# Performance work log

Hardware: AMD Instinct MI355X
Metric: run time of the kernel (lower is better)

The kernel has to match this reference:

```python
import jax, jax.numpy as jnp
import numpy as np

N_NODES = 100000
N_EDGES = 3200000
IN_C, HID_C, OUT_C = 64, 64, 32


def setup_inputs() -> dict:
    key = jax.random.key(0)
    ks = jax.random.split(key, 8)
    x = jax.random.normal(ks[0], (N_NODES, IN_C), dtype=jnp.float32)
    edge_index = jax.random.randint(ks[1], (2, N_EDGES), 0, N_NODES, dtype=jnp.int64)
    s1 = 1.0 / np.sqrt(IN_C)
    s2 = 1.0 / np.sqrt(HID_C)
    W1l = jax.random.uniform(ks[2], (IN_C, HID_C), jnp.float32, -s1, s1)
    b1l = jnp.zeros((HID_C,), jnp.float32)
    W1r = jax.random.uniform(ks[3], (IN_C, HID_C), jnp.float32, -s1, s1)
    W2l = jax.random.uniform(ks[4], (HID_C, OUT_C), jnp.float32, -s2, s2)
    b2l = jnp.zeros((OUT_C,), jnp.float32)
    W2r = jax.random.uniform(ks[5], (HID_C, OUT_C), jnp.float32, -s2, s2)
    return {"x": x, "edge_index": edge_index, "W1l": W1l, "b1l": b1l,
            "W1r": W1r, "W2l": W2l, "b2l": b2l, "W2r": W2r}


def _sage_conv(x, src, dst, Wl, bl, Wr):
    # mean-aggregate source features onto destination nodes
    msg = x[src]                                              # [E, d] gather
    summed = jax.ops.segment_sum(msg, dst, num_segments=N_NODES)
    deg = jax.ops.segment_sum(jnp.ones((src.shape[0],), x.dtype), dst,
                              num_segments=N_NODES)
    agg = summed / jnp.maximum(deg, 1.0)[:, None]             # [N, d]
    return agg @ Wl + bl + x @ Wr                             # lin_l(agg)+lin_r(x)


def reference(x, edge_index, W1l, b1l, W1r, W2l, b2l, W2r):
    src, dst = edge_index[0], edge_index[1]
    h = jax.nn.relu(_sage_conv(x, src, dst, W1l, b1l, W1r))
    # dropout is identity in eval mode
    return _sage_conv(h, src, dst, W2l, b2l, W2r)
```

## Files before the change

### kernel.cpp

```cpp
#include <hip/hip_runtime.h>
#include <hip/hip_bf16.h>

#define N_NODES 100000
#define N_EDGES 3200000
#define NBKT 391
#define BKT_CAP 10240

typedef __hip_bfloat16 bf16;
typedef unsigned int uint;
typedef __attribute__((ext_vector_type(8))) short bf16x8;
typedef __attribute__((ext_vector_type(4))) float f32x4;

__device__ __forceinline__ float b2f(bf16 v) { return __bfloat162float(v); }

__device__ __forceinline__ float bits2f(unsigned short w) {
    union { unsigned short u; bf16 b; } c;
    c.u = w;
    return __bfloat162float(c.b);
}
__device__ __forceinline__ unsigned short f2bits(float f) {
    return (unsigned short)(__float_as_uint(f) >> 16);
}
__device__ __forceinline__ unsigned short f2bf_bits(float f) {
    bf16 b = __float2bfloat16(f);
    unsigned short u;
    __builtin_memcpy(&u, &b, 2);
    return u;
}

__device__ __forceinline__ int get_idx(const void* ei, long long pos, int is64) {
    if (is64) return (int)((const long long*)ei)[pos];
    return ((const int*)ei)[pos];
}
__device__ __forceinline__ float get_f(const void* p, long long pos, int isbf) {
    if (isbf) return b2f(((const bf16*)p)[pos]);
    return ((const float*)p)[pos];
}

__global__ void detect_kernel(const void* __restrict__ x,
                              const void* __restrict__ ei,
                              int* __restrict__ flags) {
    int lane = threadIdx.x;
    const unsigned short* xw = (const unsigned short*)x;
    float v = bits2f(xw[2 * lane]);
    bool plaus = (v == v) && fabsf(v) > 1e-3f && fabsf(v) < 1e2f;
    unsigned long long m1 = __ballot(plaus);
    const int* iw = (const int*)ei;
    bool z = (iw[2 * lane + 1] == 0);
    unsigned long long m2 = __ballot(z);
    if (lane == 0) {
        flags[0] = (__popcll(m1) >= 32) ? 1 : 0;
        flags[1] = (__popcll(m2) == 64) ? 1 : 0;
    }
}

__global__ __launch_bounds__(256) void scatterA_kernel(
    const void* __restrict__ ei, int* __restrict__ bucket_cursor,
    uint* __restrict__ bucket_data, const int* __restrict__ flags) {
    __shared__ int lhist[NBKT];
    __shared__ int lbase[NBKT];
    int is64 = flags[1];
    int t = threadIdx.x;
    int chunk0 = blockIdx.x * 8192;
    int dreg[32];

    for (int i = t; i < NBKT; i += 256) lhist[i] = 0;
    __syncthreads();
#pragma unroll
    for (int j = 0; j < 32; j++) {
        int e = chunk0 + j * 256 + t;
        int d = -1;
        if (e < N_EDGES) {
            d = get_idx(ei, (long long)N_EDGES + e, is64);
            atomicAdd(&lhist[d >> 8], 1);
        }
        dreg[j] = d;
    }
    __syncthreads();
    for (int i = t; i < NBKT; i += 256) {
        int c = lhist[i];
        lbase[i] = c ? atomicAdd(&bucket_cursor[i], c) : 0;
        lhist[i] = 0;
    }
    __syncthreads();
#pragma unroll
    for (int j = 0; j < 32; j++) {
        int e = chunk0 + j * 256 + t;
        int d = dreg[j];
        if (d >= 0) {
            int s = get_idx(ei, e, is64);
            int b = d >> 8;
            int o = lbase[b] + atomicAdd(&lhist[b], 1);
            if (o < BKT_CAP)
                bucket_data[(long long)b * BKT_CAP + o] = ((uint)(d & 255) << 17) | (uint)s;
        }
    }
}

__global__ void scanBuckets_kernel(const int* __restrict__ cnt,
                                   int* __restrict__ base) {
    __shared__ int buf[512];
    int t = threadIdx.x;
    int v = (t < NBKT) ? cnt[t] : 0;
    buf[t] = v;
    __syncthreads();
    for (int off = 1; off < 512; off <<= 1) {
        int add = (t >= off) ? buf[t - off] : 0;
        __syncthreads();
        buf[t] += add;
        __syncthreads();
    }
    if (t < NBKT) base[t] = buf[t] - v;
}

__global__ __launch_bounds__(256) void csrB_kernel(
    const int* __restrict__ bucket_cnt, const int* __restrict__ bucket_base,
    const uint* __restrict__ bucket_data, int* __restrict__ csr_src,
    int* __restrict__ row_start) {
    __shared__ int lh[256];
    __shared__ int buf[256];
    int b = blockIdx.x;
    int t = threadIdx.x;
    int cnt = bucket_cnt[b];
    if (cnt > BKT_CAP) cnt = BKT_CAP;
    int base = bucket_base[b];
    const uint* bd = bucket_data + (long long)b * BKT_CAP;

    lh[t] = 0;
    __syncthreads();
    for (int i = t; i < cnt; i += 256) atomicAdd(&lh[bd[i] >> 17], 1);
    __syncthreads();
    int v = lh[t];
    buf[t] = v;
    __syncthreads();
    for (int off = 1; off < 256; off <<= 1) {
        int add = (t >= off) ? buf[t - off] : 0;
        __syncthreads();
        buf[t] += add;
        __syncthreads();
    }
    int excl = buf[t] - v;
    int g = (b << 8) + t;
    if (g < N_NODES) row_start[g] = base + excl;
    lh[t] = excl;
    __syncthreads();
    for (int i = t; i < cnt; i += 256) {
        uint e = bd[i];
        int o = atomicAdd(&lh[e >> 17], 1);
        csr_src[base + o] = (int)(e & 0x1FFFFu);
    }
    if (b == 0 && t == 0) row_start[N_NODES] = N_EDGES;
}

__global__ __launch_bounds__(256) void gather1_kernel(
    const void* __restrict__ x, const int* __restrict__ row_start,
    const int* __restrict__ csr_src, bf16* __restrict__ aggbuf,
    const int* __restrict__ flags) {
    int isbf = flags[0];
    int t = threadIdx.x;
    int lane = t & 63;
    int gw = (blockIdx.x * 256 + t) >> 6;
    int nw = (gridDim.x * 256) >> 6;
    int e8 = lane >> 3, q8 = lane & 7;
    int e4 = lane >> 4, q16 = lane & 15;
    const uint4* xr4 = (const uint4*)x;

    for (int p = gw; p * 2 < N_NODES; p += nw) {
        int na = p * 2, nb = p * 2 + 1;
        int sa = row_start[na], ea = row_start[na + 1];
        int sb = row_start[nb], eb = row_start[nb + 1];
        int da = ea - sa, db = eb - sb;
        int maxd = max(da, db);
        float accA[8] = {0, 0, 0, 0, 0, 0, 0, 0};
        float accB[8] = {0, 0, 0, 0, 0, 0, 0, 0};
        float avA = 0.0f, avB = 0.0f;
        if (isbf) {
            for (int off = 0; off < maxd; off += 32) {
                int iA0 = sa + off + e8, iA1 = iA0 + 8, iA2 = iA0 + 16, iA3 = iA0 + 24;
                int iB0 = sb + off + e8, iB1 = iB0 + 8, iB2 = iB0 + 16, iB3 = iB0 + 24;
                int sA0 = (iA0 < ea) ? csr_src[iA0] : -1;
                int sA1 = (iA1 < ea) ? csr_src[iA1] : -1;
                int sA2 = (iA2 < ea) ? csr_src[iA2] : -1;
                int sA3 = (iA3 < ea) ? csr_src[iA3] : -1;
                int sB0 = (iB0 < eb) ? csr_src[iB0] : -1;
                int sB1 = (iB1 < eb) ? csr_src[iB1] : -1;
                int sB2 = (iB2 < eb) ? csr_src[iB2] : -1;
                int sB3 = (iB3 < eb) ? csr_src[iB3] : -1;
                uint4 vA0 = {0,0,0,0}, vA1 = {0,0,0,0}, vA2 = {0,0,0,0}, vA3 = {0,0,0,0};
                uint4 vB0 = {0,0,0,0}, vB1 = {0,0,0,0}, vB2 = {0,0,0,0}, vB3 = {0,0,0,0};
                if (sA0 >= 0) vA0 = xr4[sA0 * 8 + q8];
                if (sA1 >= 0) vA1 = xr4[sA1 * 8 + q8];
                if (sA2 >= 0) vA2 = xr4[sA2 * 8 + q8];
                if (sA3 >= 0) vA3 = xr4[sA3 * 8 + q8];
                if (sB0 >= 0) vB0 = xr4[sB0 * 8 + q8];
                if (sB1 >= 0) vB1 = xr4[sB1 * 8 + q8];
                if (sB2 >= 0) vB2 = xr4[sB2 * 8 + q8];
                if (sB3 >= 0) vB3 = xr4[sB3 * 8 + q8];
                accA[0] += __uint_as_float(vA0.x << 16) + __uint_as_float(vA1.x << 16)
                         + __uint_as_float(vA2.x << 16) + __uint_as_float(vA3.x << 16);
                accA[1] += __uint_as_float(vA0.x & 0xffff0000u) + __uint_as_float(vA1.x & 0xffff0000u)
                         + __uint_as_float(vA2.x & 0xffff0000u) + __uint_as_float(vA3.x & 0xffff0000u);
                accA[2] += __uint_as_float(vA0.y << 16) + __uint_as_float(vA1.y << 16)
                         + __uint_as_float(vA2.y << 16) + __uint_as_float(vA3.y << 16);
                accA[3] += __uint_as_float(vA0.y & 0xffff0000u) + __uint_as_float(vA1.y & 0xffff0000u)
                         + __uint_as_float(vA2.y & 0xffff0000u) + __uint_as_float(vA3.y & 0xffff0000u);
                accA[4] += __uint_as_float(vA0.z << 16) + __uint_as_float(vA1.z << 16)
                         + __uint_as_float(vA2.z << 16) + __uint_as_float(vA3.z << 16);
                accA[5] += __uint_as_float(vA0.z & 0xffff0000u) + __uint_as_float(vA1.z & 0xffff0000u)
                         + __uint_as_float(vA2.z & 0xffff0000u) + __uint_as_float(vA3.z & 0xffff0000u);
                accA[6] += __uint_as_float(vA0.w << 16) + __uint_as_float(vA1.w << 16)
                         + __uint_as_float(vA2.w << 16) + __uint_as_float(vA3.w << 16);
                accA[7] += __uint_as_float(vA0.w & 0xffff0000u) + __uint_as_float(vA1.w & 0xffff0000u)
                         + __uint_as_float(vA2.w & 0xffff0000u) + __uint_as_float(vA3.w & 0xffff0000u);
                accB[0] += __uint_as_float(vB0.x << 16) + __uint_as_float(vB1.x << 16)
                         + __uint_as_float(vB2.x << 16) + __uint_as_float(vB3.x << 16);
                accB[1] += __uint_as_float(vB0.x & 0xffff0000u) + __uint_as_float(vB1.x & 0xffff0000u)
                         + __uint_as_float(vB2.x & 0xffff0000u) + __uint_as_float(vB3.x & 0xffff0000u);
                accB[2] += __uint_as_float(vB0.y << 16) + __uint_as_float(vB1.y << 16)
                         + __uint_as_float(vB2.y << 16) + __uint_as_float(vB3.y << 16);
                accB[3] += __uint_as_float(vB0.y & 0xffff0000u) + __uint_as_float(vB1.y & 0xffff0000u)
                         + __uint_as_float(vB2.y & 0xffff0000u) + __uint_as_float(vB3.y & 0xffff0000u);
                accB[4] += __uint_as_float(vB0.z << 16) + __uint_as_float(vB1.z << 16)
                         + __uint_as_float(vB2.z << 16) + __uint_as_float(vB3.z << 16);
                accB[5] += __uint_as_float(vB0.z & 0xffff0000u) + __uint_as_float(vB1.z & 0xffff0000u)
                         + __uint_as_float(vB2.z & 0xffff0000u) + __uint_as_float(vB3.z & 0xffff0000u);
                accB[6] += __uint_as_float(vB0.w << 16) + __uint_as_float(vB1.w << 16)
                         + __uint_as_float(vB2.w << 16) + __uint_as_float(vB3.w << 16);
                accB[7] += __uint_as_float(vB0.w & 0xffff0000u) + __uint_as_float(vB1.w & 0xffff0000u)
                         + __uint_as_float(vB2.w & 0xffff0000u) + __uint_as_float(vB3.w & 0xffff0000u);
            }
#pragma unroll
            for (int mm = 8; mm <= 32; mm <<= 1)
#pragma unroll
                for (int k = 0; k < 8; k++) {
                    accA[k] += __shfl_xor(accA[k], mm, 64);
                    accB[k] += __shfl_xor(accB[k], mm, 64);
                }
#pragma unroll
            for (int k = 0; k < 8; k++) {
                float vA = __shfl(accA[k], lane >> 3, 64);
                float vB = __shfl(accB[k], lane >> 3, 64);
                avA = ((lane & 7) == k) ? vA : avA;
                avB = ((lane & 7) == k) ? vB : avB;
            }
        } else {
            const uint4* xf = (const uint4*)x;
            for (int off = 0; off < maxd; off += 16) {
                int iA0 = sa + off + e4, iA1 = iA0 + 4, iA2 = iA0 + 8, iA3 = iA0 + 12;
                int iB0 = sb + off + e4, iB1 = iB0 + 4, iB2 = iB0 + 8, iB3 = iB0 + 12;
                int sA0 = (iA0 < ea) ? csr_src[iA0] : -1;
                int sA1 = (iA1 < ea) ? csr_src[iA1] : -1;
                int sA2 = (iA2 < ea) ? csr_src[iA2] : -1;
                int sA3 = (iA3 < ea) ? csr_src[iA3] : -1;
                int sB0 = (iB0 < eb) ? csr_src[iB0] : -1;
                int sB1 = (iB1 < eb) ? csr_src[iB1] : -1;
                int sB2 = (iB2 < eb) ? csr_src[iB2] : -1;
                int sB3 = (iB3 < eb) ? csr_src[iB3] : -1;
                uint4 vA0 = {0,0,0,0}, vA1 = {0,0,0,0}, vA2 = {0,0,0,0}, vA3 = {0,0,0,0};
                uint4 vB0 = {0,0,0,0}, vB1 = {0,0,0,0}, vB2 = {0,0,0,0}, vB3 = {0,0,0,0};
                if (sA0 >= 0) vA0 = xf[sA0 * 16 + q16];
                if (sA1 >= 0) vA1 = xf[sA1 * 16 + q16];
                if (sA2 >= 0) vA2 = xf[sA2 * 16 + q16];
                if (sA3 >= 0) vA3 = xf[sA3 * 16 + q16];
                if (sB0 >= 0) vB0 = xf[sB0 * 16 + q16];
                if (sB1 >= 0) vB1 = xf[sB1 * 16 + q16];
                if (sB2 >= 0) vB2 = xf[sB2 * 16 + q16];
                if (sB3 >= 0) vB3 = xf[sB3 * 16 + q16];
                accA[0] += __uint_as_float(vA0.x) + __uint_as_float(vA1.x)
                         + __uint_as_float(vA2.x) + __uint_as_float(vA3.x);
                accA[1] += __uint_as_float(vA0.y) + __uint_as_float(vA1.y)
                         + __uint_as_float(vA2.y) + __uint_as_float(vA3.y);
                accA[2] += __uint_as_float(vA0.z) + __uint_as_float(vA1.z)
                         + __uint_as_float(vA2.z) + __uint_as_float(vA3.z);
                accA[3] += __uint_as_float(vA0.w) + __uint_as_float(vA1.w)
                         + __uint_as_float(vA2.w) + __uint_as_float(vA3.w);
                accB[0] += __uint_as_float(vB0.x) + __uint_as_float(vB1.x)
                         + __uint_as_float(vB2.x) + __uint_as_float(vB3.x);
                accB[1] += __uint_as_float(vB0.y) + __uint_as_float(vB1.y)
                         + __uint_as_float(vB2.y) + __uint_as_float(vB3.y);
                accB[2] += __uint_as_float(vB0.z) + __uint_as_float(vB1.z)
                         + __uint_as_float(vB2.z) + __uint_as_float(vB3.z);
                accB[3] += __uint_as_float(vB0.w) + __uint_as_float(vB1.w)
                         + __uint_as_float(vB2.w) + __uint_as_float(vB3.w);
            }
#pragma unroll
            for (int mm = 16; mm <= 32; mm <<= 1)
#pragma unroll
                for (int k = 0; k < 4; k++) {
                    accA[k] += __shfl_xor(accA[k], mm, 64);
                    accB[k] += __shfl_xor(accB[k], mm, 64);
                }
#pragma unroll
            for (int k = 0; k < 4; k++) {
                float vA = __shfl(accA[k], lane >> 2, 64);
                float vB = __shfl(accB[k], lane >> 2, 64);
                avA = ((lane & 3) == k) ? vA : avA;
                avB = ((lane & 3) == k) ? vB : avB;
            }
        }
        avA *= 1.0f / fmaxf((float)da, 1.0f);
        avB *= 1.0f / fmaxf((float)db, 1.0f);
        aggbuf[(long long)na * 64 + lane] = __float2bfloat16(avA);
        aggbuf[(long long)nb * 64 + lane] = __float2bfloat16(avB);
    }
}

__global__ __launch_bounds__(256) void gemm1_kernel(
    const void* __restrict__ x, const bf16* __restrict__ aggbuf,
    const void* __restrict__ W1l, const void* __restrict__ b1l,
    const void* __restrict__ W1r, const void* __restrict__ W2l,
    const void* __restrict__ b2l, const void* __restrict__ W2r,
    bf16* __restrict__ zbuf, bf16* __restrict__ rbuf,
    const int* __restrict__ flags) {
    __shared__ __align__(16) unsigned short sW1t[64][136];
    __shared__ __align__(16) unsigned short sA[64][136];
    __shared__ __align__(16) unsigned short sW2t[64][72];
    __shared__ __align__(16) unsigned short sH[64][72];
    __shared__ float sB1[64];
    __shared__ float sB2[32];

    int isbf = flags[0];
    int t = threadIdx.x;
    int n0 = blockIdx.x * 64;

    for (int i = t; i < 64 * 128; i += 256) {
        int n = i & 63, k = i >> 6;
        unsigned short v;
        if (isbf)
            v = (k < 64) ? ((const unsigned short*)W1l)[k * 64 + n]
                         : ((const unsigned short*)W1r)[(k - 64) * 64 + n];
        else
            v = f2bits((k < 64) ? ((const float*)W1l)[k * 64 + n]
                                : ((const float*)W1r)[(k - 64) * 64 + n]);
        sW1t[n][k] = v;
    }
    for (int i = t; i < 64 * 64; i += 256) {
        int n = i & 63, k = i >> 6;
        unsigned short v;
        if (isbf)
            v = (n < 32) ? ((const unsigned short*)W2l)[k * 32 + n]
                         : ((const unsigned short*)W2r)[k * 32 + (n - 32)];
        else
            v = f2bits((n < 32) ? ((const float*)W2l)[k * 32 + n]
                                : ((const float*)W2r)[k * 32 + (n - 32)]);
        sW2t[n][k] = v;
    }
    if (t < 64) sB1[t] = get_f(b1l, t, isbf);
    if (t < 32) sB2[t] = get_f(b2l, t, isbf);

    const uint4* ag4 = (const uint4*)aggbuf;
    if (isbf) {
        const uint4* x4 = (const uint4*)x;
        for (int i = t; i < 64 * 16; i += 256) {
            int m = i >> 4, c = i & 15;
            int nn = min(n0 + m, N_NODES - 1);
            uint4 v = (c < 8) ? ag4[(long long)nn * 8 + c]
                              : x4[(long long)nn * 8 + (c - 8)];
            *(uint4*)&sA[m][c * 8] = v;
        }
    } else {
        for (int i = t; i < 64 * 8; i += 256) {
            int m = i >> 3, c = i & 7;
            int nn = min(n0 + m, N_NODES - 1);
            *(uint4*)&sA[m][c * 8] = ag4[(long long)nn * 8 + c];
        }
        const float* xf = (const float*)x;
        for (int i = t; i < 64 * 64; i += 256) {
            int m = i >> 6, c = i & 63;
            int nn = min(n0 + m, N_NODES - 1);
            sA[m][64 + c] = f2bf_bits(xf[(long long)nn * 64 + c]);
        }
    }
    __syncthreads();

    int w = t >> 6, lane = t & 63;
    int mbase = w * 16;
    int q = lane >> 4, r15 = lane & 15;
    f32x4 acc1[4] = {{0,0,0,0},{0,0,0,0},{0,0,0,0},{0,0,0,0}};
#pragma unroll
    for (int ks = 0; ks < 4; ks++) {
        bf16x8 afrag = *(const bf16x8*)&sA[mbase + r15][ks * 32 + q * 8];
#pragma unroll
        for (int nt = 0; nt < 4; nt++) {
            bf16x8 bfrag = *(const bf16x8*)&sW1t[nt * 16 + r15][ks * 32 + q * 8];
            acc1[nt] = __builtin_amdgcn_mfma_f32_16x16x32_bf16(afrag, bfrag, acc1[nt], 0, 0, 0);
        }
    }
#pragma unroll
    for (int nt = 0; nt < 4; nt++) {
        int col = nt * 16 + r15;
        float bias = sB1[col];
#pragma unroll
        for (int rr = 0; rr < 4; rr++) {
            int m = mbase + q * 4 + rr;
            sH[m][col] = f2bf_bits(fmaxf(acc1[nt][rr] + bias, 0.0f));
        }
    }
    __syncthreads();

    f32x4 acc2[4] = {{0,0,0,0},{0,0,0,0},{0,0,0,0},{0,0,0,0}};
#pragma unroll
    for (int ks = 0; ks < 2; ks++) {
        bf16x8 afrag = *(const bf16x8*)&sH[mbase + r15][ks * 32 + q * 8];
#pragma unroll
        for (int nt = 0; nt < 4; nt++) {
            bf16x8 bfrag = *(const bf16x8*)&sW2t[nt * 16 + r15][ks * 32 + q * 8];
            acc2[nt] = __builtin_amdgcn_mfma_f32_16x16x32_bf16(afrag, bfrag, acc2[nt], 0, 0, 0);
        }
    }
#pragma unroll
    for (int nt = 0; nt < 4; nt++) {
        int col = nt * 16 + r15;
#pragma unroll
        for (int rr = 0; rr < 4; rr++) {
            int m = mbase + q * 4 + rr;
            int n = n0 + m;
            if (n < N_NODES) {
                float v = acc2[nt][rr];
                if (col < 32)
                    zbuf[(long long)n * 32 + col] = __float2bfloat16(v);
                else
                    rbuf[(long long)n * 32 + (col - 32)] = __float2bfloat16(v + sB2[col - 32]);
            }
        }
    }
}

__global__ void node2_kernel(const int* __restrict__ row_start,
                             const int* __restrict__ csr_src,
                             const bf16* __restrict__ z,
                             const bf16* __restrict__ rbuf,
                             void* __restrict__ out,
                             const int* __restrict__ flags) {
    int isbf = flags[0];
    int t = threadIdx.x;
    int lane = t & 63;
    int e = lane >> 2, q = lane & 3;
    int gw = (blockIdx.x * blockDim.x + t) >> 6;
    int nwaves = (gridDim.x * blockDim.x) >> 6;
    const uint4* zr = (const uint4*)z;

    for (int p = gw; p * 2 < N_NODES; p += nwaves) {
        int na = p * 2, nb = p * 2 + 1;
        int sa = row_start[na], ea = row_start[na + 1];
        int sb = row_start[nb], eb = row_start[nb + 1];
        float accA[8] = {0, 0, 0, 0, 0, 0, 0, 0};
        float accB[8] = {0, 0, 0, 0, 0, 0, 0, 0};
        int da = ea - sa, db = eb - sb;
        int maxd = max(da, db);
        for (int off = 0; off < maxd; off += 32) {
            int iA0 = sa + off + e, iA1 = iA0 + 16;
            int iB0 = sb + off + e, iB1 = iB0 + 16;
            int sA0 = (iA0 < ea) ? csr_src[iA0] : -1;
            int sA1 = (iA1 < ea) ? csr_src[iA1] : -1;
            int sB0 = (iB0 < eb) ? csr_src[iB0] : -1;
            int sB1 = (iB1 < eb) ? csr_src[iB1] : -1;
            uint4 vA0 = {0,0,0,0}, vA1 = {0,0,0,0}, vB0 = {0,0,0,0}, vB1 = {0,0,0,0};
            if (sA0 >= 0) vA0 = zr[sA0 * 4 + q];
            if (sA1 >= 0) vA1 = zr[sA1 * 4 + q];
            if (sB0 >= 0) vB0 = zr[sB0 * 4 + q];
            if (sB1 >= 0) vB1 = zr[sB1 * 4 + q];
            accA[0] += __uint_as_float(vA0.x << 16) + __uint_as_float(vA1.x << 16);
            accA[1] += __uint_as_float(vA0.x & 0xffff0000u) + __uint_as_float(vA1.x & 0xffff0000u);
            accA[2] += __uint_as_float(vA0.y << 16) + __uint_as_float(vA1.y << 16);
            accA[3] += __uint_as_float(vA0.y & 0xffff0000u) + __uint_as_float(vA1.y & 0xffff0000u);
            accA[4] += __uint_as_float(vA0.z << 16) + __uint_as_float(vA1.z << 16);
            accA[5] += __uint_as_float(vA0.z & 0xffff0000u) + __uint_as_float(vA1.z & 0xffff0000u);
            accA[6] += __uint_as_float(vA0.w << 16) + __uint_as_float(vA1.w << 16);
            accA[7] += __uint_as_float(vA0.w & 0xffff0000u) + __uint_as_float(vA1.w & 0xffff0000u);
            accB[0] += __uint_as_float(vB0.x << 16) + __uint_as_float(vB1.x << 16);
            accB[1] += __uint_as_float(vB0.x & 0xffff0000u) + __uint_as_float(vB1.x & 0xffff0000u);
            accB[2] += __uint_as_float(vB0.y << 16) + __uint_as_float(vB1.y << 16);
            accB[3] += __uint_as_float(vB0.y & 0xffff0000u) + __uint_as_float(vB1.y & 0xffff0000u);
            accB[4] += __uint_as_float(vB0.z << 16) + __uint_as_float(vB1.z << 16);
            accB[5] += __uint_as_float(vB0.z & 0xffff0000u) + __uint_as_float(vB1.z & 0xffff0000u);
            accB[6] += __uint_as_float(vB0.w << 16) + __uint_as_float(vB1.w << 16);
            accB[7] += __uint_as_float(vB0.w & 0xffff0000u) + __uint_as_float(vB1.w & 0xffff0000u);
        }
#pragma unroll
        for (int m = 4; m <= 32; m <<= 1)
#pragma unroll
            for (int k = 0; k < 8; k++) {
                accA[k] += __shfl_xor(accA[k], m, 64);
                accB[k] += __shfl_xor(accB[k], m, 64);
            }
        float svA = 0.0f, svB = 0.0f;
#pragma unroll
        for (int k = 0; k < 8; k++) {
            float vA = __shfl(accA[k], lane >> 3, 64);
            float vB = __shfl(accB[k], lane >> 3, 64);
            svA = ((lane & 7) == k) ? vA : svA;
            svB = ((lane & 7) == k) ? vB : svB;
        }
        if (lane < 32) {
            float invA = 1.0f / fmaxf((float)da, 1.0f);
            float invB = 1.0f / fmaxf((float)db, 1.0f);
            float valA = svA * invA + b2f(rbuf[(long long)na * 32 + lane]);
            float valB = svB * invB + b2f(rbuf[(long long)nb * 32 + lane]);
            if (isbf) {
                ((bf16*)out)[(long long)na * 32 + lane] = __float2bfloat16(valA);
                ((bf16*)out)[(long long)nb * 32 + lane] = __float2bfloat16(valB);
            } else {
                ((float*)out)[(long long)na * 32 + lane] = valA;
                ((float*)out)[(long long)nb * 32 + lane] = valB;
            }
        }
    }
}

extern "C" void kernel_launch(void* const* d_in, const int* in_sizes, int n_in,
                              void* d_out, int out_size, void* d_ws, size_t ws_size,
                              hipStream_t stream) {
    const void* x = d_in[0];
    const void* ei = d_in[1];
    const void* W1l = d_in[2];
    const void* b1l = d_in[3];
    const void* W1r = d_in[4];
    const void* W2l = d_in[5];
    const void* b2l = d_in[6];
    const void* W2r = d_in[7];

    char* ws = (char*)d_ws;
    uint* bucket_data = (uint*)ws;
    bf16* aggbuf = (bf16*)ws;
    int* csr_src = (int*)(ws + 16015424);
    int* row_start = (int*)(ws + 28815424);
    int* bucket_cursor = (int*)(ws + 29215488);
    int* bucket_base = (int*)(ws + 29217088);
    bf16* zbuf = (bf16*)(ws + 29218688);
    bf16* rbuf = (bf16*)(ws + 35618688);
    int* flags = (int*)(ws + 42018688);

    hipMemsetAsync(bucket_cursor, 0, NBKT * 4, stream);

    detect_kernel<<<1, 64, 0, stream>>>(x, ei, flags);
    scatterA_kernel<<<NBKT, 256, 0, stream>>>(ei, bucket_cursor, bucket_data, flags);
    scanBuckets_kernel<<<1, 512, 0, stream>>>(bucket_cursor, bucket_base);
    csrB_kernel<<<NBKT, 256, 0, stream>>>(bucket_cursor, bucket_base, bucket_data,
                                          csr_src, row_start);
    gather1_kernel<<<3125, 256, 0, stream>>>(x, row_start, csr_src, aggbuf, flags);
    gemm1_kernel<<<1563, 256, 0, stream>>>(x, aggbuf, W1l, b1l, W1r, W2l, b2l,
                                           W2r, zbuf, rbuf, flags);
    node2_kernel<<<8192, 256, 0, stream>>>(row_start, csr_src, zbuf, rbuf, d_out,
                                           flags);
}
```

Baseline: 355.1 us.

## Quantize node features to int8 with per-row scales before layer-1 gather

Adds a kernel that quantizes each row of x to int8 with a per-node fp32 scale, and rewrites the layer-1 gather to read 64-byte int8 rows plus a scale instead of bf16 or fp32 rows. The goal is to cut the bytes moved by the random gather over 3.2M edges, which is memory-bound. In exchange it adds one extra pass over x, more unpacking arithmetic and a wider shuffle reduction, and it loses precision in the aggregated features. That approximation may not meet the reference tolerance.

```diff
diff --git a/kernel.cpp b/kernel.cpp
--- a/kernel.cpp
+++ b/kernel.cpp
@@ -36,6 +36,26 @@
     if (isbf) return b2f(((const bf16*)p)[pos]);
     return ((const float*)p)[pos];
 }
+
+#define UNP16(v, fs, A)                                                        \
+    {                                                                          \
+        A[0] += (float)((int)((v).x << 24) >> 24) * (fs);                      \
+        A[1] += (float)((int)((v).x << 16) >> 24) * (fs);                      \
+        A[2] += (float)((int)((v).x << 8) >> 24) * (fs);                       \
+        A[3] += (float)(((int)(v).x) >> 24) * (fs);                            \
+        A[4] += (float)((int)((v).y << 24) >> 24) * (fs);                      \
+        A[5] += (float)((int)((v).y << 16) >> 24) * (fs);                      \
+        A[6] += (float)((int)((v).y << 8) >> 24) * (fs);                       \
+        A[7] += (float)(((int)(v).y) >> 24) * (fs);                            \
+        A[8] += (float)((int)((v).z << 24) >> 24) * (fs);                      \
+        A[9] += (float)((int)((v).z << 16) >> 24) * (fs);                      \
+        A[10] += (float)((int)((v).z << 8) >> 24) * (fs);                      \
+        A[11] += (float)(((int)(v).z) >> 24) * (fs);                           \
+        A[12] += (float)((int)((v).w << 24) >> 24) * (fs);                     \
+        A[13] += (float)((int)((v).w << 16) >> 24) * (fs);                     \
+        A[14] += (float)((int)((v).w << 8) >> 24) * (fs);                      \
+        A[15] += (float)(((int)(v).w) >> 24) * (fs);                           \
+    }
 
 __global__ void detect_kernel(const void* __restrict__ x,
                               const void* __restrict__ ei,
@@ -54,6 +74,26 @@
     }
 }
 
+__global__ __launch_bounds__(256) void quantX_kernel(
+    const void* __restrict__ x, char* __restrict__ x8,
+    float* __restrict__ scl, const int* __restrict__ flags) {
+    int isbf = flags[0];
+    int t = threadIdx.x;
+    int lane = t & 63;
+    int gw = (blockIdx.x * 256 + t) >> 6;
+    int nw = (gridDim.x * 256) >> 6;
+    for (int n = gw; n < N_NODES; n += nw) {
+        float v = get_f(x, (long long)n * 64 + lane, isbf);
+        float a = fabsf(v);
+#pragma unroll
+        for (int mm = 1; mm <= 32; mm <<= 1) a = fmaxf(a, __shfl_xor(a, mm, 64));
+        float inv = (a > 0.0f) ? 127.0f / a : 0.0f;
+        int q = __float2int_rn(v * inv);
+        x8[(long long)n * 64 + lane] = (char)q;
+        if (lane == 0) scl[n] = a * (1.0f / 127.0f);
+    }
+}
+
 __global__ __launch_bounds__(256) void scatterA_kernel(
     const void* __restrict__ ei, int* __restrict__ bucket_cursor,
     uint* __restrict__ bucket_data, const int* __restrict__ flags) {
@@ -153,150 +193,60 @@
 }
 
 __global__ __launch_bounds__(256) void gather1_kernel(
-    const void* __restrict__ x, const int* __restrict__ row_start,
-    const int* __restrict__ csr_src, bf16* __restrict__ aggbuf,
-    const int* __restrict__ flags) {
-    int isbf = flags[0];
+    const char* __restrict__ x8, const float* __restrict__ scl,
+    const int* __restrict__ row_start, const int* __restrict__ csr_src,
+    bf16* __restrict__ aggbuf) {
     int t = threadIdx.x;
     int lane = t & 63;
     int gw = (blockIdx.x * 256 + t) >> 6;
     int nw = (gridDim.x * 256) >> 6;
-    int e8 = lane >> 3, q8 = lane & 7;
-    int e4 = lane >> 4, q16 = lane & 15;
-    const uint4* xr4 = (const uint4*)x;
+    int e = lane >> 2, q = lane & 3;
+    const uint4* xq = (const uint4*)x8;
 
     for (int p = gw; p * 2 < N_NODES; p += nw) {
-        int na = p * 2, nb = p * 2 + 1;
+        int na = p * 2, nb = na + 1;
         int sa = row_start[na], ea = row_start[na + 1];
         int sb = row_start[nb], eb = row_start[nb + 1];
         int da = ea - sa, db = eb - sb;
         int maxd = max(da, db);
-        float accA[8] = {0, 0, 0, 0, 0, 0, 0, 0};
-        float accB[8] = {0, 0, 0, 0, 0, 0, 0, 0};
+        float aA[16] = {0, 0, 0, 0, 0, 0, 0, 0, 0, 0, 0, 0, 0, 0, 0, 0};
+        float aB[16] = {0, 0, 0, 0, 0, 0, 0, 0, 0, 0, 0, 0, 0, 0, 0, 0};
+        for (int off = 0; off < maxd; off += 32) {
+            int iA0 = sa + off + e, iA1 = iA0 + 16;
+            int iB0 = sb + off + e, iB1 = iB0 + 16;
+            int sA0 = (iA0 < ea) ? csr_src[iA0] : -1;
+            int sA1 = (iA1 < ea) ? csr_src[iA1] : -1;
+            int sB0 = (iB0 < eb) ? csr_src[iB0] : -1;
+            int sB1 = (iB1 < eb) ? csr_src[iB1] : -1;
+            float fA0 = (sA0 >= 0) ? scl[sA0] : 0.0f;
+            float fA1 = (sA1 >= 0) ? scl[sA1] : 0.0f;
+            float fB0 = (sB0 >= 0) ? scl[sB0] : 0.0f;
+            float fB1 = (sB1 >= 0) ? scl[sB1] : 0.0f;
+            uint4 vA0 = {0, 0, 0, 0}, vA1 = {0, 0, 0, 0};
+            uint4 vB0 = {0, 0, 0, 0}, vB1 = {0, 0, 0, 0};
+            if (sA0 >= 0) vA0 = xq[sA0 * 4 + q];
+            if (sA1 >= 0) vA1 = xq[sA1 * 4 + q];
+            if (sB0 >= 0) vB0 = xq[sB0 * 4 + q];
+            if (sB1 >= 0) vB1 = xq[sB1 * 4 + q];
+            UNP16(vA0, fA0, aA);
+            UNP16(vA1, fA1, aA);
+            UNP16(vB0, fB0, aB);
+            UNP16(vB1, fB1, aB);
+        }
+#pragma unroll
+        for (int mm = 4; mm <= 32; mm <<= 1)
+#pragma unroll
+            for (int k = 0; k < 16; k++) {
+                aA[k] += __shfl_xor(aA[k], mm, 64);
+                aB[k] += __shfl_xor(aB[k], mm, 64);
+            }
         float avA = 0.0f, avB = 0.0f;
-        if (isbf) {
-            for (int off = 0; off < maxd; off += 32) {
-                int iA0 = sa + off + e8, iA1 = iA0 + 8, iA2 = iA0 + 16, iA3 = iA0 + 24;
-                int iB0 = sb + off + e8, iB1 = iB0 + 8, iB2 = iB0 + 16, iB3 = iB0 + 24;
-                int sA0 = (iA0 < ea) ? csr_src[iA0] : -1;
-                int sA1 = (iA1 < ea) ? csr_src[iA1] : -1;
-                int sA2 = (iA2 < ea) ? csr_src[iA2] : -1;
-                int sA3 = (iA3 < ea) ? csr_src[iA3] : -1;
-                int sB0 = (iB0 < eb) ? csr_src[iB0] : -1;
-                int sB1 = (iB1 < eb) ? csr_src[iB1] : -1;
-                int sB2 = (iB2 < eb) ? csr_src[iB2] : -1;
-                int sB3 = (iB3 < eb) ? csr_src[iB3] : -1;
-                uint4 vA0 = {0,0,0,0}, vA1 = {0,0,0,0}, vA2 = {0,0,0,0}, vA3 = {0,0,0,0};
-                uint4 vB0 = {0,0,0,0}, vB1 = {0,0,0,0}, vB2 = {0,0,0,0}, vB3 = {0,0,0,0};
-                if (sA0 >= 0) vA0 = xr4[sA0 * 8 + q8];
-                if (sA1 >= 0) vA1 = xr4[sA1 * 8 + q8];
-                if (sA2 >= 0) vA2 = xr4[sA2 * 8 + q8];
-                if (sA3 >= 0) vA3 = xr4[sA3 * 8 + q8];
-                if (sB0 >= 0) vB0 = xr4[sB0 * 8 + q8];
-                if (sB1 >= 0) vB1 = xr4[sB1 * 8 + q8];
-                if (sB2 >= 0) vB2 = xr4[sB2 * 8 + q8];
-                if (sB3 >= 0) vB3 = xr4[sB3 * 8 + q8];
-                accA[0] += __uint_as_float(vA0.x << 16) + __uint_as_float(vA1.x << 16)
-                         + __uint_as_float(vA2.x << 16) + __uint_as_float(vA3.x << 16);
-                accA[1] += __uint_as_float(vA0.x & 0xffff0000u) + __uint_as_float(vA1.x & 0xffff0000u)
-                         + __uint_as_float(vA2.x & 0xffff0000u) + __uint_as_float(vA3.x & 0xffff0000u);
-                accA[2] += __uint_as_float(vA0.y << 16) + __uint_as_float(vA1.y << 16)
-                         + __uint_as_float(vA2.y << 16) + __uint_as_float(vA3.y << 16);
-                accA[3] += __uint_as_float(vA0.y & 0xffff0000u) + __uint_as_float(vA1.y & 0xffff0000u)
-                         + __uint_as_float(vA2.y & 0xffff0000u) + __uint_as_float(vA3.y & 0xffff0000u);
-                accA[4] += __uint_as_float(vA0.z << 16) + __uint_as_float(vA1.z << 16)
-                         + __uint_as_float(vA2.z << 16) + __uint_as_float(vA3.z << 16);
-                accA[5] += __uint_as_float(vA0.z & 0xffff0000u) + __uint_as_float(vA1.z & 0xffff0000u)
-                         + __uint_as_float(vA2.z & 0xffff0000u) + __uint_as_float(vA3.z & 0xffff0000u);
-                accA[6] += __uint_as_float(vA0.w << 16) + __uint_as_float(vA1.w << 16)
-                         + __uint_as_float(vA2.w << 16) + __uint_as_float(vA3.w << 16);
-                accA[7] += __uint_as_float(vA0.w & 0xffff0000u) + __uint_as_float(vA1.w & 0xffff0000u)
-                         + __uint_as_float(vA2.w & 0xffff0000u) + __uint_as_float(vA3.w & 0xffff0000u);
-                accB[0] += __uint_as_float(vB0.x << 16) + __uint_as_float(vB1.x << 16)
-                         + __uint_as_float(vB2.x << 16) + __uint_as_float(vB3.x << 16);
-                accB[1] += __uint_as_float(vB0.x & 0xffff0000u) + __uint_as_float(vB1.x & 0xffff0000u)
-                         + __uint_as_float(vB2.x & 0xffff0000u) + __uint_as_float(vB3.x & 0xffff0000u);
-                accB[2] += __uint_as_float(vB0.y << 16) + __uint_as_float(vB1.y << 16)
-                         + __uint_as_float(vB2.y << 16) + __uint_as_float(vB3.y << 16);
-                accB[3] += __uint_as_float(vB0.y & 0xffff0000u) + __uint_as_float(vB1.y & 0xffff0000u)
-                         + __uint_as_float(vB2.y & 0xffff0000u) + __uint_as_float(vB3.y & 0xffff0000u);
-                accB[4] += __uint_as_float(vB0.z << 16) + __uint_as_float(vB1.z << 16)
-                         + __uint_as_float(vB2.z << 16) + __uint_as_float(vB3.z << 16);
-                accB[5] += __uint_as_float(vB0.z & 0xffff0000u) + __uint_as_float(vB1.z & 0xffff0000u)
-                         + __uint_as_float(vB2.z & 0xffff0000u) + __uint_as_float(vB3.z & 0xffff0000u);
-                accB[6] += __uint_as_float(vB0.w << 16) + __uint_as_float(vB1.w << 16)
-                         + __uint_as_float(vB2.w << 16) + __uint_as_float(vB3.w << 16);
-                accB[7] += __uint_as_float(vB0.w & 0xffff0000u) + __uint_as_float(vB1.w & 0xffff0000u)
-                         + __uint_as_float(vB2.w & 0xffff0000u) + __uint_as_float(vB3.w & 0xffff0000u);
-            }
-#pragma unroll
-            for (int mm = 8; mm <= 32; mm <<= 1)
-#pragma unroll
-                for (int k = 0; k < 8; k++) {
-                    accA[k] += __shfl_xor(accA[k], mm, 64);
-                    accB[k] += __shfl_xor(accB[k], mm, 64);
-                }
-#pragma unroll
-            for (int k = 0; k < 8; k++) {
-                float vA = __shfl(accA[k], lane >> 3, 64);
-                float vB = __shfl(accB[k], lane >> 3, 64);
-                avA = ((lane & 7) == k) ? vA : avA;
-                avB = ((lane & 7) == k) ? vB : avB;
-            }
-        } else {
-            const uint4* xf = (const uint4*)x;
-            for (int off = 0; off < maxd; off += 16) {
-                int iA0 = sa + off + e4, iA1 = iA0 + 4, iA2 = iA0 + 8, iA3 = iA0 + 12;
-                int iB0 = sb + off + e4, iB1 = iB0 + 4, iB2 = iB0 + 8, iB3 = iB0 + 12;
-                int sA0 = (iA0 < ea) ? csr_src[iA0] : -1;
-                int sA1 = (iA1 < ea) ? csr_src[iA1] : -1;
-                int sA2 = (iA2 < ea) ? csr_src[iA2] : -1;
-                int sA3 = (iA3 < ea) ? csr_src[iA3] : -1;
-                int sB0 = (iB0 < eb) ? csr_src[iB0] : -1;
-                int sB1 = (iB1 < eb) ? csr_src[iB1] : -1;
-                int sB2 = (iB2 < eb) ? csr_src[iB2] : -1;
-                int sB3 = (iB3 < eb) ? csr_src[iB3] : -1;
-                uint4 vA0 = {0,0,0,0}, vA1 = {0,0,0,0}, vA2 = {0,0,0,0}, vA3 = {0,0,0,0};
-                uint4 vB0 = {0,0,0,0}, vB1 = {0,0,0,0}, vB2 = {0,0,0,0}, vB3 = {0,0,0,0};
-                if (sA0 >= 0) vA0 = xf[sA0 * 16 + q16];
-                if (sA1 >= 0) vA1 = xf[sA1 * 16 + q16];
-                if (sA2 >= 0) vA2 = xf[sA2 * 16 + q16];
-                if (sA3 >= 0) vA3 = xf[sA3 * 16 + q16];
-                if (sB0 >= 0) vB0 = xf[sB0 * 16 + q16];
-                if (sB1 >= 0) vB1 = xf[sB1 * 16 + q16];
-                if (sB2 >= 0) vB2 = xf[sB2 * 16 + q16];
-                if (sB3 >= 0) vB3 = xf[sB3 * 16 + q16];
-                accA[0] += __uint_as_float(vA0.x) + __uint_as_float(vA1.x)
-                         + __uint_as_float(vA2.x) + __uint_as_float(vA3.x);
-                accA[1] += __uint_as_float(vA0.y) + __uint_as_float(vA1.y)
-                         + __uint_as_float(vA2.y) + __uint_as_float(vA3.y);
-                accA[2] += __uint_as_float(vA0.z) + __uint_as_float(vA1.z)
-                         + __uint_as_float(vA2.z) + __uint_as_float(vA3.z);
-                accA[3] += __uint_as_float(vA0.w) + __uint_as_float(vA1.w)
-                         + __uint_as_float(vA2.w) + __uint_as_float(vA3.w);
-                accB[0] += __uint_as_float(vB0.x) + __uint_as_float(vB1.x)
-                         + __uint_as_float(vB2.x) + __uint_as_float(vB3.x);
-                accB[1] += __uint_as_float(vB0.y) + __uint_as_float(vB1.y)
-                         + __uint_as_float(vB2.y) + __uint_as_float(vB3.y);
-                accB[2] += __uint_as_float(vB0.z) + __uint_as_float(vB1.z)
-                         + __uint_as_float(vB2.z) + __uint_as_float(vB3.z);
-                accB[3] += __uint_as_float(vB0.w) + __uint_as_float(vB1.w)
-                         + __uint_as_float(vB2.w) + __uint_as_float(vB3.w);
-            }
-#pragma unroll
-            for (int mm = 16; mm <= 32; mm <<= 1)
-#pragma unroll
-                for (int k = 0; k < 4; k++) {
-                    accA[k] += __shfl_xor(accA[k], mm, 64);
-                    accB[k] += __shfl_xor(accB[k], mm, 64);
-                }
-#pragma unroll
-            for (int k = 0; k < 4; k++) {
-                float vA = __shfl(accA[k], lane >> 2, 64);
-                float vB = __shfl(accB[k], lane >> 2, 64);
-                avA = ((lane & 3) == k) ? vA : avA;
-                avB = ((lane & 3) == k) ? vB : avB;
-            }
+#pragma unroll
+        for (int k = 0; k < 16; k++) {
+            float vA = __shfl(aA[k], lane >> 4, 64);
+            float vB = __shfl(aB[k], lane >> 4, 64);
+            avA = ((lane & 15) == k) ? vA : avA;
+            avB = ((lane & 15) == k) ? vB : avB;
         }
         avA *= 1.0f / fmaxf((float)da, 1.0f);
         avB *= 1.0f / fmaxf((float)db, 1.0f);
@@ -530,15 +480,18 @@
     bf16* zbuf = (bf16*)(ws + 29218688);
     bf16* rbuf = (bf16*)(ws + 35618688);
     int* flags = (int*)(ws + 42018688);
+    char* x8 = (char*)(ws + 42018752);
+    float* scl = (float*)(ws + 48418752);
 
     hipMemsetAsync(bucket_cursor, 0, NBKT * 4, stream);
 
     detect_kernel<<<1, 64, 0, stream>>>(x, ei, flags);
+    quantX_kernel<<<6250, 256, 0, stream>>>(x, x8, scl, flags);
     scatterA_kernel<<<NBKT, 256, 0, stream>>>(ei, bucket_cursor, bucket_data, flags);
     scanBuckets_kernel<<<1, 512, 0, stream>>>(bucket_cursor, bucket_base);
     csrB_kernel<<<NBKT, 256, 0, stream>>>(bucket_cursor, bucket_base, bucket_data,
                                           csr_src, row_start);
-    gather1_kernel<<<3125, 256, 0, stream>>>(x, row_start, csr_src, aggbuf, flags);
+    gather1_kernel<<<3125, 256, 0, stream>>>(x8, scl, row_start, csr_src, aggbuf);
     gemm1_kernel<<<1563, 256, 0, stream>>>(x, aggbuf, W1l, b1l, W1r, W2l, b2l,
                                            W2r, zbuf, rbuf, flags);
     node2_kernel<<<8192, 256, 0, stream>>>(row_start, csr_src, zbuf, rbuf, d_out,
```

New measurement: 367.3 us. +3.4%, slower.
